# Kernel tuning notes

Measured on AMD Instinct MI355X. Metric: run time of the kernel, lower is better.

The kernel has to match this reference:

```python
import jax, jax.numpy as jnp
import numpy as np

N = 50000        # nodes
E = 400000       # edges
SC = 64          # scalar (l=0) channels
VC = 32          # vector (l=1) channels
DIM = SC + 3 * VC  # 160
NB = 64          # radial basis functions
CUTOFF = 5.0
EPS = 1e-5


def _edge_rot_mat(edge_vec, edge_rand):
    # init_edge_rot_mat: build per-edge frame aligning edge dir with canonical axis
    dist = jnp.sqrt(jnp.sum(edge_vec ** 2, axis=1, keepdims=True))
    nx = edge_vec / dist
    ev2 = edge_rand - 0.5
    ev2 = ev2 / jnp.sqrt(jnp.sum(ev2 ** 2, axis=1, keepdims=True))
    ev2b = jnp.stack([-ev2[:, 1], ev2[:, 0], ev2[:, 2]], axis=1)
    ev2c = jnp.stack([ev2[:, 0], -ev2[:, 2], ev2[:, 1]], axis=1)
    dot = lambda a: jnp.abs(jnp.sum(a * nx, axis=1, keepdims=True))
    ev2 = jnp.where(dot(ev2) > dot(ev2b), ev2b, ev2)
    ev2 = jnp.where(dot(ev2) > dot(ev2c), ev2c, ev2)
    nz = jnp.cross(nx, ev2)
    nz = nz / jnp.sqrt(jnp.sum(nz ** 2, axis=1, keepdims=True))
    ny = jnp.cross(nx, nz)
    ny = ny / jnp.sqrt(jnp.sum(ny ** 2, axis=1, keepdims=True))
    # edge_rot_mat_inv columns = [nz, nx, -ny]; R = inv^T -> rows = [nz, nx, -ny]
    return jnp.stack([nz, nx, -ny], axis=1)  # [E,3,3]


def setup_inputs() -> dict:
    key = jax.random.key(0)
    ks = jax.random.split(key, 10)
    x = jax.random.normal(ks[0], (N, DIM), dtype=jnp.float32)
    pos = jax.random.normal(ks[1], (N, 3), dtype=jnp.float32)
    src = jax.random.randint(ks[2], (E,), 0, N)
    off = jax.random.randint(ks[3], (E,), 1, N)
    dst = (src + off) % N  # no self loops -> nonzero edge vectors
    edge_index = jnp.stack([src, dst], axis=0).astype(jnp.int64)
    edge_rand = jax.random.uniform(ks[4], (E, 3), dtype=jnp.float32)
    W0 = jax.random.normal(ks[5], (SC, SC), dtype=jnp.float32)
    W1 = jax.random.normal(ks[6], (VC, VC), dtype=jnp.float32)
    rbf_centers = jnp.linspace(0.0, CUTOFF, NB).astype(jnp.float32)
    rbf_widths = 0.5 * jnp.ones((NB,), dtype=jnp.float32)
    edge_proj_w = 0.1 * jax.random.normal(ks[7], (NB, 1), dtype=jnp.float32)
    edge_proj_b = jnp.zeros((1,), dtype=jnp.float32)
    ln_gamma = jnp.ones((SC,), dtype=jnp.float32) + 0.1 * jax.random.normal(ks[8], (SC,), dtype=jnp.float32)
    ln_beta = 0.1 * jax.random.normal(ks[9], (SC,), dtype=jnp.float32)
    return {"x": x, "pos": pos, "edge_index": edge_index, "edge_rand": edge_rand,
            "W0": W0, "W1": W1, "rbf_centers": rbf_centers, "rbf_widths": rbf_widths,
            "edge_proj_w": edge_proj_w, "edge_proj_b": edge_proj_b,
            "ln_gamma": ln_gamma, "ln_beta": ln_beta}


def reference(x, pos, edge_index, edge_rand, W0, W1, rbf_centers, rbf_widths,
              edge_proj_w, edge_proj_b, ln_gamma, ln_beta):
    src, dst = edge_index[0], edge_index[1]
    edge_vec = pos[src] - pos[dst]                       # [E,3]
    dist = jnp.sqrt(jnp.sum(edge_vec ** 2, axis=1))      # [E]
    # rotation matrices are detached in the original
    R = jax.lax.stop_gradient(_edge_rot_mat(edge_vec, edge_rand))  # [E,3,3]

    # radial basis (gaussian) with cosine cutoff envelope
    d = dist[:, None]                                    # [E,1]
    rbf = jnp.exp(-0.5 * ((d - rbf_centers) / rbf_widths) ** 2)  # [E,NB]
    cut = jnp.where(d <= CUTOFF, 0.5 * (jnp.cos(jnp.pi * d / CUTOFF) + 1.0), 0.0)
    rbf = rbf * cut                                      # [E,NB]

    # gather source features, split irreps 64x0e + 32x1e
    h = x[src]                                           # [E,DIM]
    h0 = h[:, :SC]                                       # [E,SC]
    h1 = h[:, SC:].reshape(-1, VC, 3)                    # [E,VC,3]

    # rotate l=1 block into the edge-aligned frame (Wigner-D for l=1 is R)
    h1r = jnp.einsum('eij,ecj->eci', R, h1)

    # SO2 convolution: per-l channel mixing (o3.Linear, 1/sqrt(fan_in) path norm)
    m0 = (h0 @ W0) / np.sqrt(SC)                         # [E,SC]
    m1 = jnp.einsum('ecj,cd->edj', h1r, W1) / np.sqrt(VC)  # [E,VC,3]

    # edge modulation: global mean of sigmoid(edge_proj(rbf)) (scalar, as in source)
    edge_w = jnp.mean(jax.nn.sigmoid(rbf @ edge_proj_w + edge_proj_b))
    m0 = m0 * edge_w
    m1 = m1 * edge_w

    # rotate l=1 back with R^T
    m1b = jnp.einsum('eji,ecj->eci', R, m1)
    msg = jnp.concatenate([m0, m1b.reshape(-1, 3 * VC)], axis=1)  # [E,DIM]

    # scatter-sum aggregation over destination nodes
    agg = jax.ops.segment_sum(msg, dst, num_segments=x.shape[0])  # [N,DIM]

    # EquivariantLayerNormV2: LayerNorm on l=0 slice only
    s = agg[:, :SC]
    mu = jnp.mean(s, axis=-1, keepdims=True)
    var = jnp.mean((s - mu) ** 2, axis=-1, keepdims=True)
    s_ln = (s - mu) / jnp.sqrt(var + EPS) * ln_gamma + ln_beta

    # S2Activation: SiLU on l=0 slice, identity on l=1
    s_act = jax.nn.silu(s_ln)
    return jnp.concatenate([s_act, agg[:, SC:]], axis=1)  # [N,DIM]
```

## Files before the change

kernel.cpp:

```cpp
#include <hip/hip_runtime.h>

#define N_NODES 50000
#define N_EDGES 400000
#define DIM 160
#define NB 64
#define CUTOFF 5.0f
#define LN_EPS 1e-5f
#define PI_F 3.14159265358979323846f

#define SLOT_STRIDE 64
#define DEG_STRIDE 8

#define WS_DEG   16
#define WS_PKT   (WS_DEG + N_NODES * DEG_STRIDE)
#define WS_POS4  (WS_PKT + 4 * NB)
#define WS_ESRC  (WS_POS4 + 4 * N_NODES)

__global__ __launch_bounds__(256) void prep(
    const float* __restrict__ pos, const float* __restrict__ centers,
    const float* __restrict__ widths, const float* __restrict__ proj_w,
    int* __restrict__ degp, float4* __restrict__ pkt,
    float4* __restrict__ pos4, float* __restrict__ ew_accum)
{
    const int i = blockIdx.x * blockDim.x + threadIdx.x;
    if (i < 16) ((int*)ew_accum)[i] = 0;
    if (i < NB)
        pkt[i] = make_float4(centers[i], 1.0f / widths[i], proj_w[i], 0.0f);
    if (i < N_NODES) {
        const int4 z4 = make_int4(0, 0, 0, 0);
        ((int4*)(degp))[2 * i]     = z4;
        ((int4*)(degp))[2 * i + 1] = z4;
        pos4[i] = make_float4(pos[3 * i], pos[3 * i + 1], pos[3 * i + 2], 0.0f);
    }
}

#define EPT 4

__global__ __launch_bounds__(256) void hist_ew_fill(
    const int* __restrict__ ei, const float4* __restrict__ pos4,
    const float4* __restrict__ pkt, const float* __restrict__ proj_b,
    int* __restrict__ degp, int* __restrict__ esrc, float* __restrict__ ew_accum)
{
    const float bias = proj_b[0];
    const int base = blockIdx.x * (256 * EPT) + threadIdx.x;

    int  s[EPT], d[EPT], slot[EPT];
    bool v[EPT];
    #pragma unroll
    for (int k = 0; k < EPT; ++k) {
        const int e = base + 256 * k;
        v[k] = (e < N_EDGES);
        s[k] = v[k] ? ei[e] : 0;
        d[k] = v[k] ? ei[N_EDGES + e] : 0;
    }

    #pragma unroll
    for (int k = 0; k < EPT; ++k)
        slot[k] = v[k] ? atomicAdd(&degp[(long)d[k] * DEG_STRIDE], 1) : 0;

    float4 ps[EPT], pd[EPT];
    #pragma unroll
    for (int k = 0; k < EPT; ++k) { ps[k] = pos4[s[k]]; pd[k] = pos4[d[k]]; }

    #pragma unroll
    for (int k = 0; k < EPT; ++k)
        if (v[k] && slot[k] < SLOT_STRIDE)
            esrc[((long)d[k] << 6) + slot[k]] = s[k];

    float dist[EPT];
    #pragma unroll
    for (int k = 0; k < EPT; ++k) {
        const float dx = ps[k].x - pd[k].x;
        const float dy = ps[k].y - pd[k].y;
        const float dz = ps[k].z - pd[k].z;
        dist[k] = sqrtf(dx * dx + dy * dy + dz * dz);
    }

    float z[EPT] = {0.f, 0.f, 0.f, 0.f};
    #pragma unroll 4
    for (int b = 0; b < NB; ++b) {
        const float4 t4 = pkt[b];
        #pragma unroll
        for (int k = 0; k < EPT; ++k) {
            const float t = (dist[k] - t4.x) * t4.y;
            z[k] = fmaf(__expf(-0.5f * t * t), t4.z, z[k]);
        }
    }

    float sig = 0.0f;
    #pragma unroll
    for (int k = 0; k < EPT; ++k) {
        if (v[k]) {
            const float cut = (dist[k] <= CUTOFF)
                            ? 0.5f * (__cosf(PI_F * dist[k] * (1.0f / CUTOFF)) + 1.0f)
                            : 0.0f;
            sig += 1.0f / (1.0f + __expf(-(z[k] * cut + bias)));
        }
    }

    #pragma unroll
    for (int off = 32; off > 0; off >>= 1) sig += __shfl_xor(sig, off);
    __shared__ float red[4];
    if ((threadIdx.x & 63) == 0) red[threadIdx.x >> 6] = sig;
    __syncthreads();
    if (threadIdx.x == 0)
        atomicAdd(ew_accum, red[0] + red[1] + red[2] + red[3]);
}

#define TNODES 16

__global__ __launch_bounds__(256) void gather_node(
    const float* __restrict__ x, const int* __restrict__ degp,
    const int* __restrict__ esrc, float* __restrict__ out,
    const float* __restrict__ W0, const float* __restrict__ W1,
    const float* __restrict__ ln_gamma, const float* __restrict__ ln_beta,
    const float* __restrict__ ew_accum)
{
    __shared__ float sW0[64 * 64];
    __shared__ float sW1[32 * 32];

    const int t    = threadIdx.x;
    const int lane = t & 63;
    const int w    = t >> 6;
    const int node0 = blockIdx.x * TNODES;

    {
        const float4* w04 = (const float4*)W0;
        float4* s04 = (float4*)sW0;
        #pragma unroll
        for (int i = 0; i < 4; ++i) s04[t + 256 * i] = w04[t + 256 * i];
        ((float4*)sW1)[t] = ((const float4*)W1)[t];
    }

    #pragma unroll 1
    for (int p = 0; p < 4; p += 2) {
        const int nlA = 4 * w + p;
        const int nlB = nlA + 1;
        const int nA  = node0 + nlA;
        const int nB  = node0 + nlB;
        const long nAc = (nA < N_NODES) ? nA : 0;
        const long nBc = (nB < N_NODES) ? nB : 0;

        const int svA  = esrc[(nAc << 6) + lane];
        const int svB  = esrc[(nBc << 6) + lane];
        const int cntA = (nA < N_NODES) ? min(degp[nAc * DEG_STRIDE], SLOT_STRIDE) : 0;
        const int cntB = (nB < N_NODES) ? min(degp[nBc * DEG_STRIDE], SLOT_STRIDE) : 0;

        float4 aA = make_float4(0.f, 0.f, 0.f, 0.f);
        float4 aB = make_float4(0.f, 0.f, 0.f, 0.f);

        #define GBODY(sv, cnt, acc)                                            \
        {                                                                      \
            int j = 0;                                                         \
            for (; j + 8 <= cnt; j += 8) {                                     \
                const int s0 = __shfl(sv, j);                                  \
                const int s1 = __shfl(sv, j + 1);                              \
                const int s2 = __shfl(sv, j + 2);                              \
                const int s3 = __shfl(sv, j + 3);                              \
                const int s4 = __shfl(sv, j + 4);                              \
                const int s5 = __shfl(sv, j + 5);                              \
                const int s6 = __shfl(sv, j + 6);                              \
                const int s7 = __shfl(sv, j + 7);                              \
                if (lane < 40) {                                               \
                    const float4 v0 = ((const float4*)(x + (long)s0 * DIM))[lane]; \
                    const float4 v1 = ((const float4*)(x + (long)s1 * DIM))[lane]; \
                    const float4 v2 = ((const float4*)(x + (long)s2 * DIM))[lane]; \
                    const float4 v3 = ((const float4*)(x + (long)s3 * DIM))[lane]; \
                    const float4 v4 = ((const float4*)(x + (long)s4 * DIM))[lane]; \
                    const float4 v5 = ((const float4*)(x + (long)s5 * DIM))[lane]; \
                    const float4 v6 = ((const float4*)(x + (long)s6 * DIM))[lane]; \
                    const float4 v7 = ((const float4*)(x + (long)s7 * DIM))[lane]; \
                    acc.x += ((v0.x + v1.x) + (v2.x + v3.x)) + ((v4.x + v5.x) + (v6.x + v7.x)); \
                    acc.y += ((v0.y + v1.y) + (v2.y + v3.y)) + ((v4.y + v5.y) + (v6.y + v7.y)); \
                    acc.z += ((v0.z + v1.z) + (v2.z + v3.z)) + ((v4.z + v5.z) + (v6.z + v7.z)); \
                    acc.w += ((v0.w + v1.w) + (v2.w + v3.w)) + ((v4.w + v5.w) + (v6.w + v7.w)); \
                }                                                              \
            }                                                                  \
            for (; j + 4 <= cnt; j += 4) {                                     \
                const int s0 = __shfl(sv, j);                                  \
                const int s1 = __shfl(sv, j + 1);                              \
                const int s2 = __shfl(sv, j + 2);                              \
                const int s3 = __shfl(sv, j + 3);                              \
                if (lane < 40) {                                               \
                    const float4 v0 = ((const float4*)(x + (long)s0 * DIM))[lane]; \
                    const float4 v1 = ((const float4*)(x + (long)s1 * DIM))[lane]; \
                    const float4 v2 = ((const float4*)(x + (long)s2 * DIM))[lane]; \
                    const float4 v3 = ((const float4*)(x + (long)s3 * DIM))[lane]; \
                    acc.x += (v0.x + v1.x) + (v2.x + v3.x);                    \
                    acc.y += (v0.y + v1.y) + (v2.y + v3.y);                    \
                    acc.z += (v0.z + v1.z) + (v2.z + v3.z);                    \
                    acc.w += (v0.w + v1.w) + (v2.w + v3.w);                    \
                }                                                              \
            }                                                                  \
            for (; j < cnt; ++j) {                                             \
                const int s0 = __shfl(sv, j);                                  \
                if (lane < 40) {                                               \
                    const float4 v0 = ((const float4*)(x + (long)s0 * DIM))[lane]; \
                    acc.x += v0.x; acc.y += v0.y; acc.z += v0.z; acc.w += v0.w; \
                }                                                              \
            }                                                                  \
        }
        GBODY(svA, cntA, aA)
        GBODY(svB, cntB, aB)
        #undef GBODY

        if (lane < 40) {
            if (nA < N_NODES) *(float4*)(out + (long)nA * DIM + 4 * lane) = aA;
            if (nB < N_NODES) *(float4*)(out + (long)nB * DIM + 4 * lane) = aB;
        }
    }

    __threadfence_block();
    __syncthreads();

    const float ew   = ew_accum[0] * (1.0f / 400000.0f);
    const float s_m0 = ew * 0.125f;
    const float s_m1 = ew * 0.17677669529663687f;

    const int nl  = t >> 4;
    const int sub = t & 15;
    const int node = node0 + nl;
    const bool valid = node < N_NODES;
    float* grow = out + (long)(valid ? node : 0) * DIM;

    {
        float acc[4] = {0.f, 0.f, 0.f, 0.f};

        #pragma unroll 4
        for (int k0 = 0; k0 < 64; k0 += 4) {
            const float4 a = *(const float4*)(grow + k0);
            const float4 w0 = *(const float4*)(sW0 + (k0 + 0) * 64 + 4 * sub);
            const float4 w1 = *(const float4*)(sW0 + (k0 + 1) * 64 + 4 * sub);
            const float4 w2 = *(const float4*)(sW0 + (k0 + 2) * 64 + 4 * sub);
            const float4 w3 = *(const float4*)(sW0 + (k0 + 3) * 64 + 4 * sub);
            acc[0] = fmaf(a.x, w0.x, fmaf(a.y, w1.x, fmaf(a.z, w2.x, fmaf(a.w, w3.x, acc[0]))));
            acc[1] = fmaf(a.x, w0.y, fmaf(a.y, w1.y, fmaf(a.z, w2.y, fmaf(a.w, w3.y, acc[1]))));
            acc[2] = fmaf(a.x, w0.z, fmaf(a.y, w1.z, fmaf(a.z, w2.z, fmaf(a.w, w3.z, acc[2]))));
            acc[3] = fmaf(a.x, w0.w, fmaf(a.y, w1.w, fmaf(a.z, w2.w, fmaf(a.w, w3.w, acc[3]))));
        }

        float sum = 0.0f, ssq = 0.0f;
        #pragma unroll
        for (int j = 0; j < 4; ++j) {
            acc[j] *= s_m0;
            sum += acc[j];
            ssq = fmaf(acc[j], acc[j], ssq);
        }
        #pragma unroll
        for (int m = 1; m <= 8; m <<= 1) {
            sum += __shfl_xor(sum, m);
            ssq += __shfl_xor(ssq, m);
        }

        if (valid) {
            const float mu   = sum * (1.0f / 64.0f);
            const float var  = ssq * (1.0f / 64.0f) - mu * mu;
            const float rstd = rsqrtf(var + LN_EPS);
            const float4 g = *(const float4*)(ln_gamma + 4 * sub);
            const float4 b = *(const float4*)(ln_beta  + 4 * sub);
            const float t0 = (acc[0] - mu) * rstd * g.x + b.x;
            const float t1 = (acc[1] - mu) * rstd * g.y + b.y;
            const float t2 = (acc[2] - mu) * rstd * g.z + b.z;
            const float t3 = (acc[3] - mu) * rstd * g.w + b.w;
            float4 o;
            o.x = t0 / (1.0f + __expf(-t0));
            o.y = t1 / (1.0f + __expf(-t1));
            o.z = t2 / (1.0f + __expf(-t2));
            o.w = t3 / (1.0f + __expf(-t3));
            *(float4*)(grow + 4 * sub) = o;
        }
    }

    {
        const float* bRow = grow + 64;
        float o[6] = {0.f, 0.f, 0.f, 0.f, 0.f, 0.f};

        #pragma unroll 2
        for (int tt = 0; tt < 8; ++tt) {
            const float4 v0 = *(const float4*)(bRow + 12 * tt);
            const float4 v1 = *(const float4*)(bRow + 12 * tt + 4);
            const float4 v2 = *(const float4*)(bRow + 12 * tt + 8);
            const float a[12] = { v0.x, v0.y, v0.z, v0.w,
                                  v1.x, v1.y, v1.z, v1.w,
                                  v2.x, v2.y, v2.z, v2.w };
            #pragma unroll
            for (int r = 0; r < 4; ++r) {
                const int cp = 4 * tt + r;
                const float a0 = a[3 * r];
                const float a1 = a[3 * r + 1];
                const float a2 = a[3 * r + 2];
                const float2 wc = *(const float2*)(sW1 + cp * 32 + 2 * sub);
                o[0] = fmaf(wc.x, a0, o[0]);
                o[1] = fmaf(wc.x, a1, o[1]);
                o[2] = fmaf(wc.x, a2, o[2]);
                o[3] = fmaf(wc.y, a0, o[3]);
                o[4] = fmaf(wc.y, a1, o[4]);
                o[5] = fmaf(wc.y, a2, o[5]);
            }
        }

        if (valid) {
            float* vout = grow + 64 + 6 * sub;
            float2* vo2 = (float2*)vout;
            float2 p0, p1, p2;
            p0.x = o[0] * s_m1; p0.y = o[1] * s_m1;
            p1.x = o[2] * s_m1; p1.y = o[3] * s_m1;
            p2.x = o[4] * s_m1; p2.y = o[5] * s_m1;
            vo2[0] = p0; vo2[1] = p1; vo2[2] = p2;
        }
    }
}

extern "C" void kernel_launch(void* const* d_in, const int* in_sizes, int n_in,
                              void* d_out, int out_size, void* d_ws, size_t ws_size,
                              hipStream_t stream) {
    const float* x       = (const float*)d_in[0];
    const float* pos     = (const float*)d_in[1];
    const int*   ei      = (const int*)d_in[2];
    const float* W0      = (const float*)d_in[4];
    const float* W1      = (const float*)d_in[5];
    const float* centers = (const float*)d_in[6];
    const float* widths  = (const float*)d_in[7];
    const float* proj_w  = (const float*)d_in[8];
    const float* proj_b  = (const float*)d_in[9];
    const float* gamma   = (const float*)d_in[10];
    const float* beta    = (const float*)d_in[11];

    float* out  = (float*)d_out;
    int*   wsi  = (int*)d_ws;
    float* ew   = (float*)d_ws;
    int*   degp = wsi + WS_DEG;
    float4* pkt  = (float4*)(wsi + WS_PKT);
    float4* pos4 = (float4*)(wsi + WS_POS4);
    int*   esrc = wsi + WS_ESRC;

    const int pb = (N_NODES + 255) / 256;
    prep<<<pb, 256, 0, stream>>>(pos, centers, widths, proj_w, degp, pkt, pos4, ew);

    const int eb = (N_EDGES + 256 * EPT - 1) / (256 * EPT);
    hist_ew_fill<<<eb, 256, 0, stream>>>(ei, pos4, pkt, proj_b, degp, esrc, ew);

    const int tiles = (N_NODES + TNODES - 1) / TNODES;
    gather_node<<<tiles, 256, 0, stream>>>(x, degp, esrc, out,
                                           W0, W1, gamma, beta, ew);
}
```

Baseline: 186.0 us.

## Keep gathered node rows in shared memory and fuse the transform into the gather loop

Gathered per-node aggregates now go to a per-wave shared-memory staging buffer instead of global memory. Each wave then applies the W0/LayerNorm/SiLU and W1 transforms right away, with each half-wave handling one node. This drops the global write-then-reread round trip and the block-wide barrier between the gather and transform phases. The cost is more shared memory per block, which may lower occupancy, and narrower per-thread work in the matmuls (2 or 3 outputs per lane).

```diff
diff --git a/kernel.cpp b/kernel.cpp
--- a/kernel.cpp
+++ b/kernel.cpp
@@ -118,6 +118,7 @@
 {
     __shared__ float sW0[64 * 64];
     __shared__ float sW1[32 * 32];
+    __shared__ float sRow[4][2][160];
 
     const int t    = threadIdx.x;
     const int lane = t & 63;
@@ -131,13 +132,19 @@
         for (int i = 0; i < 4; ++i) s04[t + 256 * i] = w04[t + 256 * i];
         ((float4*)sW1)[t] = ((const float4*)W1)[t];
     }
+    __syncthreads();
+
+    const float ew   = ew_accum[0] * (1.0f / 400000.0f);
+    const float s_m0 = ew * 0.125f;
+    const float s_m1 = ew * 0.17677669529663687f;
+
+    const int half = lane >> 5;
+    const int l    = lane & 31;
 
     #pragma unroll 1
     for (int p = 0; p < 4; p += 2) {
-        const int nlA = 4 * w + p;
-        const int nlB = nlA + 1;
-        const int nA  = node0 + nlA;
-        const int nB  = node0 + nlB;
+        const int nA  = node0 + 4 * w + p;
+        const int nB  = nA + 1;
         const long nAc = (nA < N_NODES) ? nA : 0;
         const long nBc = (nB < N_NODES) ? nB : 0;
 
@@ -205,108 +212,78 @@
         #undef GBODY
 
         if (lane < 40) {
-            if (nA < N_NODES) *(float4*)(out + (long)nA * DIM + 4 * lane) = aA;
-            if (nB < N_NODES) *(float4*)(out + (long)nB * DIM + 4 * lane) = aB;
-        }
-    }
-
-    __threadfence_block();
-    __syncthreads();
-
-    const float ew   = ew_accum[0] * (1.0f / 400000.0f);
-    const float s_m0 = ew * 0.125f;
-    const float s_m1 = ew * 0.17677669529663687f;
-
-    const int nl  = t >> 4;
-    const int sub = t & 15;
-    const int node = node0 + nl;
-    const bool valid = node < N_NODES;
-    float* grow = out + (long)(valid ? node : 0) * DIM;
-
-    {
-        float acc[4] = {0.f, 0.f, 0.f, 0.f};
-
-        #pragma unroll 4
-        for (int k0 = 0; k0 < 64; k0 += 4) {
-            const float4 a = *(const float4*)(grow + k0);
-            const float4 w0 = *(const float4*)(sW0 + (k0 + 0) * 64 + 4 * sub);
-            const float4 w1 = *(const float4*)(sW0 + (k0 + 1) * 64 + 4 * sub);
-            const float4 w2 = *(const float4*)(sW0 + (k0 + 2) * 64 + 4 * sub);
-            const float4 w3 = *(const float4*)(sW0 + (k0 + 3) * 64 + 4 * sub);
-            acc[0] = fmaf(a.x, w0.x, fmaf(a.y, w1.x, fmaf(a.z, w2.x, fmaf(a.w, w3.x, acc[0]))));
-            acc[1] = fmaf(a.x, w0.y, fmaf(a.y, w1.y, fmaf(a.z, w2.y, fmaf(a.w, w3.y, acc[1]))));
-            acc[2] = fmaf(a.x, w0.z, fmaf(a.y, w1.z, fmaf(a.z, w2.z, fmaf(a.w, w3.z, acc[2]))));
-            acc[3] = fmaf(a.x, w0.w, fmaf(a.y, w1.w, fmaf(a.z, w2.w, fmaf(a.w, w3.w, acc[3]))));
-        }
-
-        float sum = 0.0f, ssq = 0.0f;
-        #pragma unroll
-        for (int j = 0; j < 4; ++j) {
-            acc[j] *= s_m0;
-            sum += acc[j];
-            ssq = fmaf(acc[j], acc[j], ssq);
-        }
-        #pragma unroll
-        for (int m = 1; m <= 8; m <<= 1) {
-            sum += __shfl_xor(sum, m);
-            ssq += __shfl_xor(ssq, m);
-        }
-
-        if (valid) {
-            const float mu   = sum * (1.0f / 64.0f);
-            const float var  = ssq * (1.0f / 64.0f) - mu * mu;
-            const float rstd = rsqrtf(var + LN_EPS);
-            const float4 g = *(const float4*)(ln_gamma + 4 * sub);
-            const float4 b = *(const float4*)(ln_beta  + 4 * sub);
-            const float t0 = (acc[0] - mu) * rstd * g.x + b.x;
-            const float t1 = (acc[1] - mu) * rstd * g.y + b.y;
-            const float t2 = (acc[2] - mu) * rstd * g.z + b.z;
-            const float t3 = (acc[3] - mu) * rstd * g.w + b.w;
-            float4 o;
-            o.x = t0 / (1.0f + __expf(-t0));
-            o.y = t1 / (1.0f + __expf(-t1));
-            o.z = t2 / (1.0f + __expf(-t2));
-            o.w = t3 / (1.0f + __expf(-t3));
-            *(float4*)(grow + 4 * sub) = o;
-        }
-    }
-
-    {
-        const float* bRow = grow + 64;
-        float o[6] = {0.f, 0.f, 0.f, 0.f, 0.f, 0.f};
-
-        #pragma unroll 2
-        for (int tt = 0; tt < 8; ++tt) {
-            const float4 v0 = *(const float4*)(bRow + 12 * tt);
-            const float4 v1 = *(const float4*)(bRow + 12 * tt + 4);
-            const float4 v2 = *(const float4*)(bRow + 12 * tt + 8);
-            const float a[12] = { v0.x, v0.y, v0.z, v0.w,
-                                  v1.x, v1.y, v1.z, v1.w,
-                                  v2.x, v2.y, v2.z, v2.w };
+            *(float4*)(&sRow[w][0][4 * lane]) = aA;
+            *(float4*)(&sRow[w][1][4 * lane]) = aB;
+        }
+
+        const int  node  = node0 + 4 * w + p + half;
+        const bool valid = node < N_NODES;
+        float* grow = out + (long)(valid ? node : 0) * DIM;
+        const float* row = &sRow[w][half][0];
+
+        {
+            float a0 = 0.f, a1 = 0.f;
+            #pragma unroll 4
+            for (int k0 = 0; k0 < 64; k0 += 4) {
+                const float4 a = *(const float4*)(row + k0);
+                const float2 q0 = *(const float2*)(sW0 + (k0 + 0) * 64 + 2 * l);
+                const float2 q1 = *(const float2*)(sW0 + (k0 + 1) * 64 + 2 * l);
+                const float2 q2 = *(const float2*)(sW0 + (k0 + 2) * 64 + 2 * l);
+                const float2 q3 = *(const float2*)(sW0 + (k0 + 3) * 64 + 2 * l);
+                a0 = fmaf(a.x, q0.x, fmaf(a.y, q1.x, fmaf(a.z, q2.x, fmaf(a.w, q3.x, a0))));
+                a1 = fmaf(a.x, q0.y, fmaf(a.y, q1.y, fmaf(a.z, q2.y, fmaf(a.w, q3.y, a1))));
+            }
+            a0 *= s_m0;
+            a1 *= s_m0;
+
+            float sum = a0 + a1;
+            float ssq = fmaf(a0, a0, a1 * a1);
             #pragma unroll
-            for (int r = 0; r < 4; ++r) {
-                const int cp = 4 * tt + r;
-                const float a0 = a[3 * r];
-                const float a1 = a[3 * r + 1];
-                const float a2 = a[3 * r + 2];
-                const float2 wc = *(const float2*)(sW1 + cp * 32 + 2 * sub);
-                o[0] = fmaf(wc.x, a0, o[0]);
-                o[1] = fmaf(wc.x, a1, o[1]);
-                o[2] = fmaf(wc.x, a2, o[2]);
-                o[3] = fmaf(wc.y, a0, o[3]);
-                o[4] = fmaf(wc.y, a1, o[4]);
-                o[5] = fmaf(wc.y, a2, o[5]);
-            }
-        }
-
-        if (valid) {
-            float* vout = grow + 64 + 6 * sub;
-            float2* vo2 = (float2*)vout;
-            float2 p0, p1, p2;
-            p0.x = o[0] * s_m1; p0.y = o[1] * s_m1;
-            p1.x = o[2] * s_m1; p1.y = o[3] * s_m1;
-            p2.x = o[4] * s_m1; p2.y = o[5] * s_m1;
-            vo2[0] = p0; vo2[1] = p1; vo2[2] = p2;
+            for (int m = 1; m <= 16; m <<= 1) {
+                sum += __shfl_xor(sum, m);
+                ssq += __shfl_xor(ssq, m);
+            }
+
+            if (valid) {
+                const float mu   = sum * (1.0f / 64.0f);
+                const float var  = ssq * (1.0f / 64.0f) - mu * mu;
+                const float rstd = rsqrtf(var + LN_EPS);
+                const float2 g = *(const float2*)(ln_gamma + 2 * l);
+                const float2 b = *(const float2*)(ln_beta  + 2 * l);
+                const float t0 = (a0 - mu) * rstd * g.x + b.x;
+                const float t1 = (a1 - mu) * rstd * g.y + b.y;
+                float2 o;
+                o.x = t0 / (1.0f + __expf(-t0));
+                o.y = t1 / (1.0f + __expf(-t1));
+                *(float2*)(grow + 2 * l) = o;
+            }
+        }
+
+        {
+            const float* vrow = row + 64;
+            float o0 = 0.f, o1 = 0.f, o2 = 0.f;
+            #pragma unroll 2
+            for (int g = 0; g < 8; ++g) {
+                const float4 v0 = *(const float4*)(vrow + 12 * g);
+                const float4 v1 = *(const float4*)(vrow + 12 * g + 4);
+                const float4 v2 = *(const float4*)(vrow + 12 * g + 8);
+                const float a[12] = { v0.x, v0.y, v0.z, v0.w,
+                                      v1.x, v1.y, v1.z, v1.w,
+                                      v2.x, v2.y, v2.z, v2.w };
+                #pragma unroll
+                for (int r = 0; r < 4; ++r) {
+                    const float wc = sW1[(4 * g + r) * 32 + l];
+                    o0 = fmaf(wc, a[3 * r],     o0);
+                    o1 = fmaf(wc, a[3 * r + 1], o1);
+                    o2 = fmaf(wc, a[3 * r + 2], o2);
+                }
+            }
+            if (valid) {
+                float* vo = grow + 64 + 3 * l;
+                vo[0] = o0 * s_m1;
+                vo[1] = o1 * s_m1;
+                vo[2] = o2 * s_m1;
+            }
         }
     }
 }
```

After: 180.7 us. 2.8% less time.
